# Performance work log

Measured on AMD Instinct MI355X. Metric: run time of the kernel, lower is better.

Reference implementation:

```python
import jax, jax.numpy as jnp
import numpy as np

OUT_H = OUT_W = 7
STRIDES = (4, 8, 16, 32)
CANON_SIZE = 224.0
CANON_LEVEL = 4.0
MIN_LEVEL, MAX_LEVEL = 2.0, 5.0


def _roi_align_level(feat, batch_idx, boxes, scale):
    # feat: [N,C,H,W]; boxes: [M,4] in image coords; sampling_ratio=1, aligned=False
    N, C, H, W = feat.shape
    x1, y1, x2, y2 = (boxes[:, i] * scale for i in range(4))
    roi_w = jnp.maximum(x2 - x1, 1.0)  # legacy (aligned=False) clamp
    roi_h = jnp.maximum(y2 - y1, 1.0)
    bin_w = roi_w / OUT_W
    bin_h = roi_h / OUT_H
    # one sample per bin at the bin center (sampling_ratio == 1)
    sx = x1[:, None] + (jnp.arange(OUT_W, dtype=feat.dtype) + 0.5) * bin_w[:, None]  # [M,OW]
    sy = y1[:, None] + (jnp.arange(OUT_H, dtype=feat.dtype) + 0.5) * bin_h[:, None]  # [M,OH]

    def _bilinear_axis(s, size):
        valid = (s >= -1.0) & (s <= size)
        sc = jnp.maximum(s, 0.0)
        low_raw = jnp.floor(sc).astype(jnp.int32)
        hi = low_raw >= size - 1
        low = jnp.where(hi, size - 1, low_raw)
        high = jnp.where(hi, size - 1, low_raw + 1)
        frac = jnp.where(hi, 0.0, sc - low_raw.astype(sc.dtype))
        return low, high, frac, valid

    xl, xh, lx, vx = _bilinear_axis(sx, W)
    yl, yh, ly, vy = _bilinear_axis(sy, H)
    b = batch_idx[:, None, None]  # [M,1,1]

    def gather(yi, xi):
        # advanced indexing -> [M,OH,OW,C]
        return feat[b, :, yi[:, :, None], xi[:, None, :]]

    hy, hx = 1.0 - ly, 1.0 - lx
    out = (gather(yl, xl) * (hy[:, :, None] * hx[:, None, :])[..., None]
           + gather(yl, xh) * (hy[:, :, None] * lx[:, None, :])[..., None]
           + gather(yh, xl) * (ly[:, :, None] * hx[:, None, :])[..., None]
           + gather(yh, xh) * (ly[:, :, None] * lx[:, None, :])[..., None])
    valid = (vy[:, :, None] & vx[:, None, :])[..., None]
    out = jnp.where(valid, out, 0.0)
    return jnp.transpose(out, (0, 3, 1, 2))  # [M,C,OH,OW]


def setup_inputs() -> dict:
    key = jax.random.key(0)
    ks = jax.random.split(key, 6)
    N, L, C = 2, 512, 256
    feats = {}
    for i, hw in enumerate((256, 128, 64, 32)):
        feats[f"feat{i}"] = jax.random.normal(ks[i], (N, C, hw, hw), dtype=jnp.float32)
    # valid boxes on a 1024x1024 image: x1y1 in [0,800), wh in [8,520)
    xy = jax.random.uniform(ks[4], (N, L, 2), dtype=jnp.float32) * 800.0
    wh = jax.random.uniform(ks[5], (N, L, 2), dtype=jnp.float32) * 512.0 + 8.0
    boxes = jnp.concatenate([xy, xy + wh], axis=-1)  # [N,L,4]
    feats["boxes"] = boxes
    return feats


def reference(feat0, feat1, feat2, feat3, boxes):
    feats = [feat0, feat1, feat2, feat3]
    N, L, _ = boxes.shape
    flat = boxes.reshape(-1, 4)  # [M,4]
    batch_idx = jnp.repeat(jnp.arange(N, dtype=jnp.int32), L)
    # assign_boxes_to_levels (note +1 in width/height as in the source)
    sizes = jnp.sqrt((flat[:, 2] - flat[:, 0] + 1.0) * (flat[:, 3] - flat[:, 1] + 1.0))
    lv = jnp.floor(CANON_LEVEL + jnp.log2(sizes / CANON_SIZE) + 1e-8)
    lv = jnp.clip(lv, MIN_LEVEL, MAX_LEVEL).astype(jnp.int32) - jnp.int32(MIN_LEVEL)
    M, C = flat.shape[0], feat0.shape[1]
    result = jnp.zeros((M, C, OUT_H, OUT_W), dtype=feat0.dtype)
    for l, (f, stride) in enumerate(zip(feats, STRIDES)):
        aligned = _roi_align_level(f, batch_idx, flat, 1.0 / stride)
        result = jnp.where((lv == l)[:, None, None, None], aligned, result)
    return result
```

## Files before the change

kernel.cpp:

```cpp
#include <hip/hip_runtime.h>
#include <math.h>

#define OUT_H 7
#define OUT_W 7
#define NBINS 49
#define CCH   256
#define ELEMS (NBINS * CCH)
#define KCH   7
#define GRIDX 8

typedef float f32x2 __attribute__((ext_vector_type(2)));
struct __attribute__((packed)) F2A { f32x2 v; } __attribute__((aligned(4)));

struct __align__(16) BoxHeader {
    unsigned long long planeBase;
    unsigned int       chanBytes;
    unsigned int       pad;
};
struct __align__(16) BinParam {
    unsigned int o0;
    unsigned int o1;
    float w0, w1;
    float w2, w3;
    unsigned int pad0, pad1;
};

__global__ void msroi_pre_kernel(const float* __restrict__ f0,
                                 const float* __restrict__ f1,
                                 const float* __restrict__ f2,
                                 const float* __restrict__ f3,
                                 const float* __restrict__ boxes,
                                 BoxHeader* __restrict__ hdrs,
                                 BinParam*  __restrict__ prm,
                                 int M, int L)
{
    int tid = blockIdx.x * blockDim.x + threadIdx.x;
    if (tid >= M * NBINS) return;
    int m   = tid / NBINS;
    int bin = tid - m * NBINS;
    int yh  = bin / OUT_W;
    int xw  = bin - yh * OUT_W;

    float bx1 = boxes[m*4+0], by1 = boxes[m*4+1];
    float bx2 = boxes[m*4+2], by2 = boxes[m*4+3];

    float sz  = sqrtf((bx2 - bx1 + 1.0f) * (by2 - by1 + 1.0f));
    float lvf = floorf(4.0f + log2f(sz / 224.0f) + 1e-8f);
    lvf = fminf(fmaxf(lvf, 2.0f), 5.0f);
    int lv = (int)lvf - 2;

    const float* feat; int H, W; float scale;
    switch (lv) {
        case 0:  feat = f0; H = 256; W = 256; scale = 0.25f;    break;
        case 1:  feat = f1; H = 128; W = 128; scale = 0.125f;   break;
        case 2:  feat = f2; H = 64;  W = 64;  scale = 0.0625f;  break;
        default: feat = f3; H = 32;  W = 32;  scale = 0.03125f; break;
    }

    if (bin == 0) {
        int b = m / L;
        BoxHeader h;
        h.planeBase = (unsigned long long)(const void*)(feat + (size_t)b * CCH * H * W);
        h.chanBytes = (unsigned int)(H * W * 4);
        h.pad = 0;
        hdrs[m] = h;
    }

    float x1 = bx1 * scale, y1 = by1 * scale;
    float x2 = bx2 * scale, y2 = by2 * scale;
    float roi_w = fmaxf(x2 - x1, 1.0f);
    float roi_h = fmaxf(y2 - y1, 1.0f);
    float bin_w = roi_w * (1.0f / OUT_W);
    float bin_h = roi_h * (1.0f / OUT_H);
    float sx = x1 + ((float)xw + 0.5f) * bin_w;
    float sy = y1 + ((float)yh + 0.5f) * bin_h;

    bool  vx  = (sx >= -1.0f) && (sx <= (float)W);
    float scx = fmaxf(sx, 0.0f);
    int   xlr = (int)floorf(scx);
    bool  hxf = xlr >= (W - 1);
    float lx  = hxf ? 0.0f : (scx - (float)xlr);
    int   xA  = hxf ? (W - 2) : xlr;
    float wxA = hxf ? 0.0f : (1.0f - lx);
    float wxB = hxf ? 1.0f : lx;

    bool  vy  = (sy >= -1.0f) && (sy <= (float)H);
    float scy = fmaxf(sy, 0.0f);
    int   ylr = (int)floorf(scy);
    bool  hyf = ylr >= (H - 1);
    int   rA  = hyf ? (H - 1) : ylr;
    int   rB  = hyf ? (H - 1) : (ylr + 1);
    float ly  = hyf ? 0.0f : (scy - (float)ylr);
    float wyA = 1.0f - ly;
    float wyB = ly;

    float vmask = (vx && vy) ? 1.0f : 0.0f;

    BinParam p;
    p.o0 = (unsigned)((rA * W + xA) * 4);
    p.o1 = (unsigned)((rB * W + xA) * 4);
    p.w0 = vmask * wyA * wxA;
    p.w1 = vmask * wyA * wxB;
    p.w2 = vmask * wyB * wxA;
    p.w3 = vmask * wyB * wxB;
    p.pad0 = 0; p.pad1 = 0;
    prm[tid] = p;
}

__global__ __launch_bounds__(256, 2)
void msroi_gather_kernel(const BoxHeader* __restrict__ hdrs,
                         const BinParam*  __restrict__ prm,
                         float* __restrict__ out)
{
    __shared__ unsigned so0[NBINS], so1[NBINS];
    __shared__ float    sw0[NBINS], sw1[NBINS], sw2[NBINS], sw3[NBINS];

    int bx = blockIdx.x;
    if (bx >= 7) return;
    int m   = blockIdx.y;
    int tid = threadIdx.x;

    if (tid < NBINS) {
        BinParam p = prm[(size_t)m * NBINS + tid];
        so0[tid] = p.o0; so1[tid] = p.o1;
        sw0[tid] = p.w0; sw1[tid] = p.w1;
        sw2[tid] = p.w2; sw3[tid] = p.w3;
    }
    __syncthreads();

    BoxHeader h = hdrs[m];
    const char* base = (const char*)h.planeBase;
    int e_base = bx * (256 * KCH) + tid;

    f32x2 r0[KCH], r1[KCH];
    float w0[KCH], w1[KCH], w2[KCH], w3[KCH];

    #pragma unroll
    for (int k = 0; k < KCH; ++k) {
        int e = e_base + k * 256;
        unsigned c   = (unsigned)e / NBINS;
        unsigned bin = (unsigned)e - c * NBINS;
        const char* plane = base + (unsigned long long)c
                                 * (unsigned long long)h.chanBytes;
        unsigned o0 = so0[bin], o1 = so1[bin];
        w0[k] = sw0[bin]; w1[k] = sw1[bin];
        w2[k] = sw2[bin]; w3[k] = sw3[bin];
        r0[k] = ((const F2A*)(plane + o0))->v;
        r1[k] = ((const F2A*)(plane + o1))->v;
    }

    size_t outBase = (size_t)m * ELEMS + (size_t)e_base;
    #pragma unroll
    for (int k = 0; k < KCH; ++k) {
        out[outBase + (size_t)k * 256] =
            r0[k].x * w0[k] + r0[k].y * w1[k] + r1[k].x * w2[k] + r1[k].y * w3[k];
    }
}

__global__ void msroi_align_kernel(const float* __restrict__ f0,
                                   const float* __restrict__ f1,
                                   const float* __restrict__ f2,
                                   const float* __restrict__ f3,
                                   const float* __restrict__ boxes,
                                   float* __restrict__ out,
                                   int M, int C, int L, int total)
{
    int idx = blockIdx.x * blockDim.x + threadIdx.x;
    if (idx >= total) return;

    int xw = idx % OUT_W;
    int t  = idx / OUT_W;
    int yh = t % OUT_H;
    t /= OUT_H;
    int c = t % C;
    int m = t / C;
    int b = m / L;

    float bx1 = boxes[m*4+0], by1 = boxes[m*4+1];
    float bx2 = boxes[m*4+2], by2 = boxes[m*4+3];

    float sz  = sqrtf((bx2 - bx1 + 1.0f) * (by2 - by1 + 1.0f));
    float lvf = floorf(4.0f + log2f(sz / 224.0f) + 1e-8f);
    lvf = fminf(fmaxf(lvf, 2.0f), 5.0f);
    int lv = (int)lvf - 2;

    const float* feat; int H, W; float scale;
    switch (lv) {
        case 0:  feat = f0; H = 256; W = 256; scale = 0.25f;    break;
        case 1:  feat = f1; H = 128; W = 128; scale = 0.125f;   break;
        case 2:  feat = f2; H = 64;  W = 64;  scale = 0.0625f;  break;
        default: feat = f3; H = 32;  W = 32;  scale = 0.03125f; break;
    }

    float x1 = bx1 * scale, y1 = by1 * scale;
    float x2 = bx2 * scale, y2 = by2 * scale;
    float roi_w = fmaxf(x2 - x1, 1.0f);
    float roi_h = fmaxf(y2 - y1, 1.0f);
    float bin_w = roi_w * (1.0f / OUT_W);
    float bin_h = roi_h * (1.0f / OUT_H);
    float sx = x1 + ((float)xw + 0.5f) * bin_w;
    float sy = y1 + ((float)yh + 0.5f) * bin_h;

    bool  vx  = (sx >= -1.0f) && (sx <= (float)W);
    float scx = fmaxf(sx, 0.0f);
    int   xlr = (int)floorf(scx);
    bool  hxf = xlr >= (W - 1);
    int   xl  = hxf ? (W - 1) : xlr;
    int   xh  = hxf ? (W - 1) : (xlr + 1);
    float lx  = hxf ? 0.0f : (scx - (float)xlr);

    bool  vy  = (sy >= -1.0f) && (sy <= (float)H);
    float scy = fmaxf(sy, 0.0f);
    int   ylr = (int)floorf(scy);
    bool  hyf = ylr >= (H - 1);
    int   yl  = hyf ? (H - 1) : ylr;
    int   yhh = hyf ? (H - 1) : (ylr + 1);
    float ly  = hyf ? 0.0f : (scy - (float)ylr);

    float val = 0.0f;
    if (vx && vy) {
        size_t base = ((size_t)b * (size_t)C + (size_t)c) * (size_t)(H * W);
        const float* p = feat + base;
        float v00 = p[(size_t)yl  * W + xl];
        float v01 = p[(size_t)yl  * W + xh];
        float v10 = p[(size_t)yhh * W + xl];
        float v11 = p[(size_t)yhh * W + xh];
        float hy = 1.0f - ly, hx = 1.0f - lx;
        val = v00 * (hy * hx) + v01 * (hy * lx) + v10 * (ly * hx) + v11 * (ly * lx);
    }
    out[idx] = val;
}

extern "C" void kernel_launch(void* const* d_in, const int* in_sizes, int n_in,
                              void* d_out, int out_size, void* d_ws, size_t ws_size,
                              hipStream_t stream) {
    const float* f0    = (const float*)d_in[0];
    const float* f1    = (const float*)d_in[1];
    const float* f2    = (const float*)d_in[2];
    const float* f3    = (const float*)d_in[3];
    const float* boxes = (const float*)d_in[4];
    float* out = (float*)d_out;

    const int N = 2;
    const int M = in_sizes[4] / 4;
    const int L = M / N;
    const int total = M * CCH * NBINS;

    size_t prmBytes = (size_t)M * NBINS * sizeof(BinParam);
    size_t hdrBytes = (size_t)M * sizeof(BoxHeader);
    size_t need = prmBytes + hdrBytes;

    if (ws_size >= need) {
        BinParam*  prm  = (BinParam*)d_ws;
        BoxHeader* hdrs = (BoxHeader*)((char*)d_ws + prmBytes);

        int preThreads = M * NBINS;
        msroi_pre_kernel<<<(preThreads + 255) / 256, 256, 0, stream>>>(
            f0, f1, f2, f3, boxes, hdrs, prm, M, L);

        dim3 grid(GRIDX, M);
        msroi_gather_kernel<<<grid, 256, 0, stream>>>(hdrs, prm, out);
    } else {
        int block = 256;
        int grid = (total + block - 1) / block;
        msroi_align_kernel<<<grid, block, 0, stream>>>(f0, f1, f2, f3, boxes, out,
                                                       M, CCH, L, total);
    }
}
```

Baseline: 49.93 us.

## Sort boxes by level and batch before gather to improve cache locality

Adds a single-block counting-sort kernel that buckets boxes by (FPN level, batch image) using a shared-memory prefix scan, producing a permutation. The gather kernel then processes boxes in this order, so consecutive workgroups read from the same feature plane and share L2/MALL-resident data. This costs an extra kernel launch and a serial scan over 1024 entries, and the output write pattern becomes scattered per box.

```diff
diff --git a/kernel.cpp b/kernel.cpp
--- a/kernel.cpp
+++ b/kernel.cpp
@@ -25,6 +25,76 @@
     unsigned int pad0, pad1;
 };
 
+__global__ __launch_bounds__(1024)
+void msroi_sort_kernel(const float* __restrict__ boxes, int M, int L,
+                       int* __restrict__ perm)
+{
+    __shared__ unsigned s0[1024], s1[1024], s2[1024], s3[1024];
+    __shared__ unsigned bases[8];
+    int t = threadIdx.x;
+
+    int bkt = -1;
+    if (t < M) {
+        float bx1 = boxes[t*4+0], by1 = boxes[t*4+1];
+        float bx2 = boxes[t*4+2], by2 = boxes[t*4+3];
+        float sz  = sqrtf((bx2 - bx1 + 1.0f) * (by2 - by1 + 1.0f));
+        float lvf = floorf(4.0f + log2f(sz / 224.0f) + 1e-8f);
+        lvf = fminf(fmaxf(lvf, 2.0f), 5.0f);
+        int lv = (int)lvf - 2;
+        int b  = t / L;
+        bkt = lv * 2 + b;
+    }
+
+    unsigned f0 = 0, f1 = 0, f2 = 0, f3 = 0;
+    if (bkt >= 0) {
+        unsigned inc = 1u << ((bkt & 1) * 16);
+        switch (bkt >> 1) {
+            case 0: f0 = inc; break;
+            case 1: f1 = inc; break;
+            case 2: f2 = inc; break;
+            default: f3 = inc; break;
+        }
+    }
+    s0[t] = f0; s1[t] = f1; s2[t] = f2; s3[t] = f3;
+    __syncthreads();
+
+    for (int off = 1; off < 1024; off <<= 1) {
+        unsigned v0 = 0, v1 = 0, v2 = 0, v3 = 0;
+        if (t >= off) { v0 = s0[t-off]; v1 = s1[t-off]; v2 = s2[t-off]; v3 = s3[t-off]; }
+        __syncthreads();
+        s0[t] += v0; s1[t] += v1; s2[t] += v2; s3[t] += v3;
+        __syncthreads();
+    }
+
+    if (t == 0) {
+        unsigned tot[8], run = 0;
+        tot[0] = s0[1023] & 0xFFFFu; tot[1] = s0[1023] >> 16;
+        tot[2] = s1[1023] & 0xFFFFu; tot[3] = s1[1023] >> 16;
+        tot[4] = s2[1023] & 0xFFFFu; tot[5] = s2[1023] >> 16;
+        tot[6] = s3[1023] & 0xFFFFu; tot[7] = s3[1023] >> 16;
+        for (int k = 0; k < 8; ++k) { bases[k] = run; run += tot[k]; }
+    }
+    __syncthreads();
+
+    if (bkt >= 0) {
+        unsigned packed;
+        switch (bkt >> 1) {
+            case 0: packed = s0[t]; break;
+            case 1: packed = s1[t]; break;
+            case 2: packed = s2[t]; break;
+            default: packed = s3[t]; break;
+        }
+        unsigned rank = ((packed >> ((bkt & 1) * 16)) & 0xFFFFu) - 1u;
+        perm[bases[bkt] + rank] = t;
+    }
+}
+
+__global__ void msroi_iota_kernel(int* __restrict__ perm, int M)
+{
+    int i = blockIdx.x * blockDim.x + threadIdx.x;
+    if (i < M) perm[i] = i;
+}
+
 __global__ void msroi_pre_kernel(const float* __restrict__ f0,
                                  const float* __restrict__ f1,
                                  const float* __restrict__ f2,
@@ -110,6 +180,7 @@
 __global__ __launch_bounds__(256, 2)
 void msroi_gather_kernel(const BoxHeader* __restrict__ hdrs,
                          const BinParam*  __restrict__ prm,
+                         const int*       __restrict__ perm,
                          float* __restrict__ out)
 {
     __shared__ unsigned so0[NBINS], so1[NBINS];
@@ -117,7 +188,7 @@
 
     int bx = blockIdx.x;
     if (bx >= 7) return;
-    int m   = blockIdx.y;
+    int m   = perm[blockIdx.y];
     int tid = threadIdx.x;
 
     if (tid < NBINS) {
@@ -246,20 +317,28 @@
     const int L = M / N;
     const int total = M * CCH * NBINS;
 
-    size_t prmBytes = (size_t)M * NBINS * sizeof(BinParam);
-    size_t hdrBytes = (size_t)M * sizeof(BoxHeader);
-    size_t need = prmBytes + hdrBytes;
+    size_t prmBytes  = (size_t)M * NBINS * sizeof(BinParam);
+    size_t hdrBytes  = (size_t)M * sizeof(BoxHeader);
+    size_t permBytes = (size_t)M * sizeof(int);
+    size_t need = prmBytes + hdrBytes + permBytes;
 
     if (ws_size >= need) {
         BinParam*  prm  = (BinParam*)d_ws;
         BoxHeader* hdrs = (BoxHeader*)((char*)d_ws + prmBytes);
+        int*       perm = (int*)((char*)d_ws + prmBytes + hdrBytes);
+
+        if (M <= 1024) {
+            msroi_sort_kernel<<<1, 1024, 0, stream>>>(boxes, M, L, perm);
+        } else {
+            msroi_iota_kernel<<<(M + 255) / 256, 256, 0, stream>>>(perm, M);
+        }
 
         int preThreads = M * NBINS;
         msroi_pre_kernel<<<(preThreads + 255) / 256, 256, 0, stream>>>(
             f0, f1, f2, f3, boxes, hdrs, prm, M, L);
 
         dim3 grid(GRIDX, M);
-        msroi_gather_kernel<<<grid, 256, 0, stream>>>(hdrs, prm, out);
+        msroi_gather_kernel<<<grid, 256, 0, stream>>>(hdrs, prm, perm, out);
     } else {
         int block = 256;
         int grid = (total + block - 1) / block;
```

Measured after the change: 51.85 us. 1.04x slower.
